# Performance work log

Hardware: AMD Instinct MI355X
Metric: run time of the kernel (lower is better)

Reference implementation:

```python
import jax, jax.numpy as jnp
import numpy as np

B, S, N, D = 8, 2048, 512, 1024
MAX_W = 32  # fixed max span width (inclusive widths 0..MAX_W-1)
MASK_FILL = -1000.0


def setup_inputs() -> dict:
    key = jax.random.key(0)
    k1, k2, k3, k4 = jax.random.split(key, 4)
    sequence_tensor = jax.random.normal(k1, (B, S, D), dtype=jnp.float32)
    starts = jax.random.randint(k2, (B, N), 0, S - MAX_W)
    widths = jax.random.randint(k3, (B, N), 0, MAX_W)  # inclusive width = widths
    span_indices = jnp.stack([starts, starts + widths], axis=-1)  # (B, N, 2)
    att_w = jax.random.normal(k4, (D, 1), dtype=jnp.float32) * 0.02
    att_b = jnp.zeros((1,), dtype=jnp.float32)
    return {"sequence_tensor": sequence_tensor, "span_indices": span_indices,
            "att_w": att_w, "att_b": att_b}


def reference(sequence_tensor, span_indices, att_w, att_b):
    dtype = sequence_tensor.dtype
    starts = span_indices[..., 0]               # (B, N)
    ends = span_indices[..., 1]                 # (B, N), inclusive
    widths = ends - starts                      # (B, N)

    rng = jnp.arange(MAX_W)                     # (W,)
    raw_idx = ends[..., None] - rng             # (B, N, W), walks backward from end
    span_mask = (rng <= widths[..., None]) & (raw_idx >= 0)  # (B, N, W)
    idx = jnp.maximum(raw_idx, 0)               # relu on indices

    # global attention logits: (B, S, 1)
    logits = sequence_tensor @ att_w + att_b

    b, n = idx.shape[0], idx.shape[1]
    flat = idx.reshape(b, n * MAX_W)            # (B, N*W)
    # gather embeddings and logits over the time axis
    span_emb = jnp.take_along_axis(sequence_tensor, flat[..., None], axis=1)
    span_emb = span_emb.reshape(b, n, MAX_W, -1)              # (B, N, W, D)
    span_logits = jnp.take_along_axis(logits[..., 0], flat, axis=1)
    span_logits = span_logits.reshape(b, n, MAX_W)            # (B, N, W)

    # memory-efficient masked softmax: fill masked logits with -1000
    masked_logits = jnp.where(span_mask, span_logits, jnp.asarray(MASK_FILL, dtype))
    attn = jax.nn.softmax(masked_logits, axis=-1)             # (B, N, W)

    # weighted-sum pooling over span positions
    return jnp.einsum('bnw,bnwd->bnd', attn, span_emb)
```

## Files before the change

### kernel.cpp

```cpp
#include <hip/hip_runtime.h>
#include <hip/hip_bf16.h>

#define B 8
#define S 2048
#define N 512
#define D 1024
#define MAX_W 32
#define MASK_FILL -1000.0f

typedef float vfloat4 __attribute__((ext_vector_type(4)));

__global__ __launch_bounds__(256) void logits_kernel(
    const float* __restrict__ seq,
    const float* __restrict__ att_w,
    const float* __restrict__ att_b,
    float* __restrict__ logits)
{
    const int row  = blockIdx.x * 4 + (threadIdx.x >> 6);
    const int lane = threadIdx.x & 63;

    const float4* rp = (const float4*)(seq + (size_t)row * D);
    const float4* wp = (const float4*)att_w;

    float acc = 0.0f;
#pragma unroll
    for (int k = 0; k < 4; ++k) {
        const float4 a = rp[lane + 64 * k];
        const float4 w = wp[lane + 64 * k];
        acc += a.x * w.x + a.y * w.y + a.z * w.z + a.w * w.w;
    }

#pragma unroll
    for (int off = 32; off > 0; off >>= 1)
        acc += __shfl_down(acc, off);

    if (lane == 0)
        logits[row] = acc + att_b[0];
}

__global__ __launch_bounds__(512) void sort_kernel(
    const int* __restrict__ spans,
    int* __restrict__ order)
{
    const int b = blockIdx.x;
    const int n = threadIdx.x;

    __shared__ unsigned short s_key[N];

    const int key = spans[2 * (b * N + n) + 1];
    s_key[n] = (unsigned short)key;
    __syncthreads();

    int rank = 0;
#pragma unroll 8
    for (int j = 0; j < N; ++j) {
        const int kj = (int)s_key[j];
        rank += (kj < key) | ((kj == key) & (j < n));
    }
    order[b * N + rank] = n;
}

__global__ __launch_bounds__(256) void pool_kernel(
    const float* __restrict__ seq,
    const int*   __restrict__ spans,
    const float* __restrict__ logits,
    const int*   __restrict__ order,
    float* __restrict__ out)
{
    const int b    = blockIdx.x & 7;
    const int rank = blockIdx.x >> 3;
    const int n    = order[b * N + rank];
    const int span = b * N + n;

    const int start = spans[2 * span + 0];
    const int end   = spans[2 * span + 1];
    const int width = end - start;

    __shared__ float s_attn[MAX_W];
    __shared__ int   s_idx[MAX_W];

    const int tid = threadIdx.x;

    if (tid < MAX_W) {
        const int w   = tid;
        const int raw = end - w;
        const bool valid = (w <= width) && (raw >= 0);
        const int idx = raw > 0 ? raw : 0;
        const float l = valid ? logits[b * S + idx] : MASK_FILL;

        float m = l;
#pragma unroll
        for (int off = 16; off > 0; off >>= 1)
            m = fmaxf(m, __shfl_down(m, off, 32));
        m = __shfl(m, 0, 32);

        const float p = __expf(l - m);

        float sum = p;
#pragma unroll
        for (int off = 16; off > 0; off >>= 1)
            sum += __shfl_down(sum, off, 32);
        sum = __shfl(sum, 0, 32);

        s_attn[w] = p / sum;
        s_idx[w]  = idx;
    }
    __syncthreads();

    const float* sb = seq + (size_t)b * S * D;
    float4 acc = make_float4(0.f, 0.f, 0.f, 0.f);

    const int cnt  = width + 1;
    const int cnt4 = (cnt + 3) & ~3;

    for (int w = 0; w < cnt4; w += 4) {
        const float a0 = s_attn[w + 0];
        const float a1 = s_attn[w + 1];
        const float a2 = s_attn[w + 2];
        const float a3 = s_attn[w + 3];
        const int   i0 = s_idx[w + 0];
        const int   i1 = s_idx[w + 1];
        const int   i2 = s_idx[w + 2];
        const int   i3 = s_idx[w + 3];

        const float4 v0 = ((const float4*)(sb + (size_t)i0 * D))[tid];
        const float4 v1 = ((const float4*)(sb + (size_t)i1 * D))[tid];
        const float4 v2 = ((const float4*)(sb + (size_t)i2 * D))[tid];
        const float4 v3 = ((const float4*)(sb + (size_t)i3 * D))[tid];

        acc.x += a0 * v0.x + a1 * v1.x + a2 * v2.x + a3 * v3.x;
        acc.y += a0 * v0.y + a1 * v1.y + a2 * v2.y + a3 * v3.y;
        acc.z += a0 * v0.z + a1 * v1.z + a2 * v2.z + a3 * v3.z;
        acc.w += a0 * v0.w + a1 * v1.w + a2 * v2.w + a3 * v3.w;
    }

    vfloat4 vacc;
    vacc.x = acc.x; vacc.y = acc.y; vacc.z = acc.z; vacc.w = acc.w;
    vfloat4* op = ((vfloat4*)(out + (size_t)span * D)) + tid;
    __builtin_nontemporal_store(vacc, op);
}

extern "C" void kernel_launch(void* const* d_in, const int* in_sizes, int n_in,
                              void* d_out, int out_size, void* d_ws, size_t ws_size,
                              hipStream_t stream)
{
    const float* seq    = (const float*)d_in[0];
    const int*   spans  = (const int*)  d_in[1];
    const float* att_w  = (const float*)d_in[2];
    const float* att_b  = (const float*)d_in[3];

    float* out    = (float*)d_out;
    float* logits = (float*)d_ws;
    int*   order  = (int*)((char*)d_ws + B * S * sizeof(float));

    logits_kernel<<<(B * S) / 4, 256, 0, stream>>>(seq, att_w, att_b, logits);
    sort_kernel<<<B, 512, 0, stream>>>(spans, order);
    pool_kernel<<<B * N, 256, 0, stream>>>(seq, spans, logits, order, out);
}
```

Before: 129.5 us.

## Fuse logits into pooling kernel, processing groups of sorted spans per block

Removes the separate logits kernel and computes logits on the fly for the sequence window covered by a group of 8 end-sorted spans, storing them in shared memory. Pooling then streams each row of the window once and accumulates into up to 8 span outputs, reusing loaded rows across overlapping spans. This trades the global logits pass and launch for redundant logit computation across blocks and fewer, larger blocks with more register pressure.

Result: slower. 162.1 us (+25.2%).

```diff
diff --git a/kernel.cpp b/kernel.cpp
--- a/kernel.cpp
+++ b/kernel.cpp
@@ -7,36 +7,9 @@
 #define D 1024
 #define MAX_W 32
 #define MASK_FILL -1000.0f
+#define G 8
 
 typedef float vfloat4 __attribute__((ext_vector_type(4)));
-
-__global__ __launch_bounds__(256) void logits_kernel(
-    const float* __restrict__ seq,
-    const float* __restrict__ att_w,
-    const float* __restrict__ att_b,
-    float* __restrict__ logits)
-{
-    const int row  = blockIdx.x * 4 + (threadIdx.x >> 6);
-    const int lane = threadIdx.x & 63;
-
-    const float4* rp = (const float4*)(seq + (size_t)row * D);
-    const float4* wp = (const float4*)att_w;
-
-    float acc = 0.0f;
-#pragma unroll
-    for (int k = 0; k < 4; ++k) {
-        const float4 a = rp[lane + 64 * k];
-        const float4 w = wp[lane + 64 * k];
-        acc += a.x * w.x + a.y * w.y + a.z * w.z + a.w * w.w;
-    }
-
-#pragma unroll
-    for (int off = 32; off > 0; off >>= 1)
-        acc += __shfl_down(acc, off);
-
-    if (lane == 0)
-        logits[row] = acc + att_b[0];
-}
 
 __global__ __launch_bounds__(512) void sort_kernel(
     const int* __restrict__ spans,
@@ -60,33 +33,83 @@
     order[b * N + rank] = n;
 }
 
-__global__ __launch_bounds__(256) void pool_kernel(
+__global__ __launch_bounds__(256) void fused_kernel(
     const float* __restrict__ seq,
     const int*   __restrict__ spans,
-    const float* __restrict__ logits,
+    const float* __restrict__ att_w,
+    const float* __restrict__ att_b,
     const int*   __restrict__ order,
     float* __restrict__ out)
 {
-    const int b    = blockIdx.x & 7;
-    const int rank = blockIdx.x >> 3;
-    const int n    = order[b * N + rank];
-    const int span = b * N + n;
+    const int b   = blockIdx.x & 7;
+    const int grp = blockIdx.x >> 3;
 
-    const int start = spans[2 * span + 0];
-    const int end   = spans[2 * span + 1];
-    const int width = end - start;
+    __shared__ int   s_n[G], s_start[G], s_end[G];
+    __shared__ int   s_lohi[2];
+    __shared__ float s_logit[S];
+    __shared__ float s_attn[G][MAX_W];
 
-    __shared__ float s_attn[MAX_W];
-    __shared__ int   s_idx[MAX_W];
+    const int tid  = threadIdx.x;
+    const int lane = tid & 63;
+    const int wid  = tid >> 6;
 
-    const int tid = threadIdx.x;
+    if (tid < G) {
+        const int rank = grp * G + tid;
+        const int n    = order[b * N + rank];
+        s_n[tid]     = n;
+        s_start[tid] = spans[2 * (b * N + n) + 0];
+        s_end[tid]   = spans[2 * (b * N + n) + 1];
+    }
+    __syncthreads();
+    if (tid == 0) {
+        int lo = s_start[0], hi = s_end[0];
+#pragma unroll
+        for (int g = 1; g < G; ++g) {
+            lo = min(lo, s_start[g]);
+            hi = max(hi, s_end[g]);
+        }
+        s_lohi[0] = lo; s_lohi[1] = hi;
+    }
+    __syncthreads();
+    const int lo = s_lohi[0], hi = s_lohi[1];
 
-    if (tid < MAX_W) {
-        const int w   = tid;
-        const int raw = end - w;
-        const bool valid = (w <= width) && (raw >= 0);
-        const int idx = raw > 0 ? raw : 0;
-        const float l = valid ? logits[b * S + idx] : MASK_FILL;
+    const float* sb = seq + (size_t)b * S * D;
+
+    {
+        const float4* wp = (const float4*)att_w;
+        const float4 w0 = wp[lane];
+        const float4 w1 = wp[lane + 64];
+        const float4 w2 = wp[lane + 128];
+        const float4 w3 = wp[lane + 192];
+        const float bias = att_b[0];
+
+        for (int s = lo + wid; s <= hi; s += 4) {
+            const float4* rp = (const float4*)(sb + (size_t)s * D);
+            const float4 a0 = rp[lane];
+            const float4 a1 = rp[lane + 64];
+            const float4 a2 = rp[lane + 128];
+            const float4 a3 = rp[lane + 192];
+            float acc = a0.x * w0.x + a0.y * w0.y + a0.z * w0.z + a0.w * w0.w
+                      + a1.x * w1.x + a1.y * w1.y + a1.z * w1.z + a1.w * w1.w
+                      + a2.x * w2.x + a2.y * w2.y + a2.z * w2.z + a2.w * w2.w
+                      + a3.x * w3.x + a3.y * w3.y + a3.z * w3.z + a3.w * w3.w;
+#pragma unroll
+            for (int off = 32; off > 0; off >>= 1)
+                acc += __shfl_down(acc, off);
+            if (lane == 0)
+                s_logit[s - lo] = acc + bias;
+        }
+    }
+    __syncthreads();
+
+    {
+        const int g = tid >> 5;
+        const int k = tid & 31;
+        const int en  = s_end[g];
+        const int wdt = en - s_start[g];
+        const bool valid = (k <= wdt);
+        const int  li = max(en - k - lo, 0);
+        const float l = valid ? s_logit[li] : MASK_FILL;
 
         float m = l;
 #pragma unroll
@@ -102,42 +125,39 @@
             sum += __shfl_down(sum, off, 32);
         sum = __shfl(sum, 0, 32);
 
-        s_attn[w] = p / sum;
-        s_idx[w]  = idx;
+        s_attn[g][k] = p / sum;
     }
     __syncthreads();
 
-    const float* sb = seq + (size_t)b * S * D;
-    float4 acc = make_float4(0.f, 0.f, 0.f, 0.f);
+    int st_r[G], en_r[G];
+#pragma unroll
+    for (int g = 0; g < G; ++g) { st_r[g] = s_start[g]; en_r[g] = s_end[g]; }
 
-    const int cnt  = width + 1;
-    const int cnt4 = (cnt + 3) & ~3;
+    float4 acc[G];
+#pragma unroll
+    for (int g = 0; g < G; ++g) acc[g] = make_float4(0.f, 0.f, 0.f, 0.f);
 
-    for (int w = 0; w < cnt4; w += 4) {
-        const float a0 = s_attn[w + 0];
-        const float a1 = s_attn[w + 1];
-        const float a2 = s_attn[w + 2];
-        const float a3 = s_attn[w + 3];
-        const int   i0 = s_idx[w + 0];
-        const int   i1 = s_idx[w + 1];
-        const int   i2 = s_idx[w + 2];
-        const int   i3 = s_idx[w + 3];
-
-        const float4 v0 = ((const float4*)(sb + (size_t)i0 * D))[tid];
-        const float4 v1 = ((const float4*)(sb + (size_t)i1 * D))[tid];
-        const float4 v2 = ((const float4*)(sb + (size_t)i2 * D))[tid];
-        const float4 v3 = ((const float4*)(sb + (size_t)i3 * D))[tid];
-
-        acc.x += a0 * v0.x + a1 * v1.x + a2 * v2.x + a3 * v3.x;
-        acc.y += a0 * v0.y + a1 * v1.y + a2 * v2.y + a3 * v3.y;
-        acc.z += a0 * v0.z + a1 * v1.z + a2 * v2.z + a3 * v3.z;
-        acc.w += a0 * v0.w + a1 * v1.w + a2 * v2.w + a3 * v3.w;
+    for (int s = lo; s <= hi; ++s) {
+        const float4 v = ((const float4*)(sb + (size_t)s * D))[tid];
+#pragma unroll
+        for (int g = 0; g < G; ++g) {
+            if (s >= st_r[g] && s <= en_r[g]) {
+                const float a = s_attn[g][en_r[g] - s];
+                acc[g].x += a * v.x;
+                acc[g].y += a * v.y;
+                acc[g].z += a * v.z;
+                acc[g].w += a * v.w;
+            }
+        }
     }
 
-    vfloat4 vacc;
-    vacc.x = acc.x; vacc.y = acc.y; vacc.z = acc.z; vacc.w = acc.w;
-    vfloat4* op = ((vfloat4*)(out + (size_t)span * D)) + tid;
-    __builtin_nontemporal_store(vacc, op);
+#pragma unroll
+    for (int g = 0; g < G; ++g) {
+        vfloat4 va;
+        va.x = acc[g].x; va.y = acc[g].y; va.z = acc[g].z; va.w = acc[g].w;
+        vfloat4* op = ((vfloat4*)(out + (size_t)(b * N + s_n[g]) * D)) + tid;
+        __builtin_nontemporal_store(va, op);
+    }
 }
 
 extern "C" void kernel_launch(void* const* d_in, const int* in_sizes, int n_in,
@@ -149,11 +169,10 @@
     const float* att_w  = (const float*)d_in[2];
     const float* att_b  = (const float*)d_in[3];
 
-    float* out    = (float*)d_out;
-    float* logits = (float*)d_ws;
-    int*   order  = (int*)((char*)d_ws + B * S * sizeof(float));
+    float* out   = (float*)d_out;
+    int*   order = (int*)d_ws;
 
-    logits_kernel<<<(B * S) / 4, 256, 0, stream>>>(seq, att_w, att_b, logits);
     sort_kernel<<<B, 512, 0, stream>>>(spans, order);
-    pool_kernel<<<B * N, 256, 0, stream>>>(seq, spans, logits, order, out);
+    fused_kernel<<<(B * N) / G, 256, 0, stream>>>(seq, spans, att_w, att_b,
+                                                  order, out);
 }
```
